# Kernel optimization log

Measured on AMD Instinct MI355X. Metric: run time of the kernel, lower is better.

Reference implementation:

```python
import jax, jax.numpy as jnp
import numpy as np

N, HIDDEN, K = 16384, 256, 5  # k=5 neighbors, first (self) dropped -> 4 hyperedge memberships per node


def _knn_hyperedges(x):
    # Mimics sklearn NearestNeighbors(k=5) + drop self (torch code detaches x here).
    xs = jax.lax.stop_gradient(x)
    n = xs.shape[0]
    sq = jnp.sum(xs * xs, axis=1)
    d2 = sq[:, None] + sq[None, :] - 2.0 * (xs @ xs.T)  # [N, N] squared distances
    d2 = d2.at[jnp.arange(n), jnp.arange(n)].set(jnp.inf)  # exclude self
    _, idx = jax.lax.top_k(-d2, K - 1)  # [N, K-1] nearest neighbors
    node_idx = jnp.repeat(jnp.arange(n), K - 1)  # hyperedge_index[0]: node i
    edge_idx = idx.reshape(-1)                   # hyperedge_index[1]: hyperedge id = neighbor id
    return node_idx, edge_idx


def _prelu(x, a):
    return jnp.where(x >= 0, x, a * x)


def _hconv(x, W, b, node_idx, edge_idx, n):
    # PyG HypergraphConv (heads=1, no attention, unit hyperedge weights):
    # out = D^{-1} H B^{-1} H^T (x W^T) + b
    xt = x @ W.T  # lin has no bias in PyG; bias added at the end
    ones = jnp.ones(node_idx.shape[0], dtype=x.dtype)
    Bdeg = jax.ops.segment_sum(ones, edge_idx, num_segments=n)  # hyperedge degree
    Binv = jnp.where(Bdeg > 0, 1.0 / Bdeg, 0.0)
    Ddeg = jax.ops.segment_sum(ones, node_idx, num_segments=n)  # node degree
    Dinv = jnp.where(Ddeg > 0, 1.0 / Ddeg, 0.0)
    # node -> hyperedge gather/scatter
    e_feat = jax.ops.segment_sum(xt[node_idx], edge_idx, num_segments=n) * Binv[:, None]
    # hyperedge -> node gather/scatter
    out = jax.ops.segment_sum(e_feat[edge_idx], node_idx, num_segments=n) * Dinv[:, None]
    return out + b


def setup_inputs() -> dict:
    key = jax.random.key(0)
    k0, k1, k2, k3 = jax.random.split(key, 4)
    x = jax.random.normal(k0, (N, HIDDEN), dtype=jnp.float32)
    edge_index = jax.random.randint(k1, (2, 65536), 0, N)  # unused by the math, kept per signature
    kaiming = np.sqrt(2.0 / HIDDEN)
    W1 = jax.random.normal(k2, (HIDDEN, HIDDEN), dtype=jnp.float32) * kaiming
    W2 = jax.random.normal(k3, (HIDDEN, HIDDEN), dtype=jnp.float32) * kaiming
    b1 = jnp.zeros((HIDDEN,), dtype=jnp.float32)
    b2 = jnp.zeros((HIDDEN,), dtype=jnp.float32)
    prelu_a = jnp.float32(0.25)  # nn.PReLU() default single shared parameter
    return {"x": x, "edge_index": edge_index, "W1": W1, "b1": b1, "W2": W2, "b2": b2, "prelu_a": prelu_a}


def reference(x, edge_index, W1, b1, W2, b2, prelu_a):
    n = x.shape[0]
    node_idx, edge_idx = _knn_hyperedges(x)
    h = _hconv(x, W1, b1, node_idx, edge_idx, n)
    h = _prelu(h, prelu_a)
    h = _hconv(h, W2, b2, node_idx, edge_idx, n)
    h = h + x  # residual
    return _prelu(h, prelu_a)
```

## Files before the change

### kernel.cpp

```cpp
#include <hip/hip_runtime.h>
#include <stdint.h>

#define NN   16384
#define HID  256
#define LDSK 264
#define NSLICE 16
#define JSL  (NN/NSLICE)
#define JT   32
#define NIT  (JSL/JT)
#define NSETS 4
#define ITILE (NSETS*64)
#define NRS  8
#define GSB  2048
#define NWV  (GSB*4)
#define FLTMAX 3.402823466e38f
#define KEYMAX 0xFFFFFFFFu
#define VBIAS 131072.0f
#define MSTRIDE 17

typedef __attribute__((ext_vector_type(8))) _Float16 f16x8;
typedef __attribute__((ext_vector_type(4))) _Float16 f16x4;
typedef __attribute__((ext_vector_type(4))) float f32x4;

typedef const __attribute__((address_space(1))) unsigned int* gAS1;
typedef __attribute__((address_space(3))) unsigned int* lAS3;

#define NXG (NN*HID/4)
#define NWG (HID*HID/4)
#define CVTB ((NXG + 2*NWG)/256)
__global__ __launch_bounds__(256) void prep_kernel(const float* __restrict__ x,
                                                   const float* __restrict__ W1,
                                                   const float* __restrict__ W2,
                                                   _Float16* __restrict__ xh,
                                                   _Float16* __restrict__ W1h,
                                                   _Float16* __restrict__ W2h,
                                                   float* __restrict__ sqf,
                                                   int* __restrict__ Bdeg){
  #pragma clang fp contract(off)
  int b = blockIdx.x;
  int g0 = b * 256 + threadIdx.x;
  if (g0 < NN) Bdeg[g0] = 0;
  if (b < CVTB){
    int g = g0;
    const float* src; _Float16* dst; int o;
    if (g < NXG)            { src = x;  dst = xh;  o = g; }
    else if (g < NXG + NWG) { src = W1; dst = W1h; o = g - NXG; }
    else                    { src = W2; dst = W2h; o = g - NXG - NWG; }
    float4 v = ((const float4*)src)[o];
    f16x4 h; h.x = (_Float16)v.x; h.y = (_Float16)v.y; h.z = (_Float16)v.z; h.w = (_Float16)v.w;
    ((f16x4*)dst)[o] = h;
  } else {
    int bb = b - CVTB;
    int lane = threadIdx.x & 63;
    int rw   = lane >> 4;
    int h    = (lane >> 3) & 1;
    int j    = lane & 7;
    int row  = (bb * 4 + (threadIdx.x >> 6)) * 4 + rw;
    const float* p = x + (size_t)row * HID + h*128 + j;
    float v0 = p[0];
    float r  = v0 * v0;
    #pragma unroll
    for (int i = 1; i < 16; ++i){ float v = p[i*8]; float m = v * v; r = r + m; }
    float t1 = r  + __shfl_xor(r,  1);
    float t2 = t1 + __shfl_xor(t1, 2);
    float t3 = t2 + __shfl_xor(t2, 4);
    float tot = t3 + __shfl_xor(t3, 8);
    if (h == 0 && j == 0) sqf[row] = tot;
  }
}

__device__ __forceinline__ void load_tile64(unsigned short* dst, const unsigned short* src, int tid){
  const uint4* s = (const uint4*)src;
  #pragma unroll
  for (int r = 0; r < 8; ++r){
    int fl  = tid + (r << 8);
    int row = fl >> 5;
    int c   = fl & 31;
    *(uint4*)&dst[row*LDSK + (c << 3)] = s[fl];
  }
}

__device__ __forceinline__ unsigned umed3(unsigned a, unsigned b, unsigned c){
  unsigned d;
  asm("v_med3_u32 %0, %1, %2, %3" : "=v"(d) : "v"(a), "v"(b), "v"(c));
  return d;
}
__device__ __forceinline__ void ins4(unsigned (&b)[4], unsigned k){
  unsigned b0 = b[0], b1 = b[1], b2 = b[2];
  b[0] = k < b0 ? k : b0;
  b[1] = umed3(k, b0, b1);
  b[2] = umed3(k, b1, b2);
  b[3] = umed3(k, b2, b[3]);
}

__global__ __launch_bounds__(256, 2) void knn_kernel(const _Float16* __restrict__ xh,
                                                     const float* __restrict__ sqf,
                                                     unsigned* __restrict__ candk,
                                                     int ibase){
  __shared__ __align__(16) unsigned short Xj[2][JT*256];
  __shared__ __align__(16) float sqj64[2][JT];

  int tid  = threadIdx.x;
  int sl   = blockIdx.x & (NSLICE-1);
  int i0   = ibase + (blockIdx.x / NSLICE) * ITILE;
  int jb0  = sl * JSL;
  int wave = tid >> 6, lane = tid & 63, quad = lane >> 4, lcol = lane & 15;

  f16x8 bfr[NSETS][8];
  #pragma unroll
  for (int s = 0; s < NSETS; ++s){
    const _Float16* br = xh + (size_t)(i0 + s*64 + wave*16 + lcol) * HID + quad*8;
    #pragma unroll
    for (int ks = 0; ks < 8; ++ks) bfr[s][ks] = *(const f16x8*)(br + ks*32);
  }

  const _Float16* gsrc[4];
  #pragma unroll
  for (int r = 0; r < 4; ++r){
    int m   = r*256 + tid;
    int row = m >> 5;
    int ch  = m & 31;
    gsrc[r] = xh + (size_t)row * HID + ((ch ^ (row & 7)) << 3);
  }

  int b0 = lcol*512 + ((quad ^ (lcol & 3)) << 4) + (((lcol >> 2) & 1) << 6);
  int b1 = b0 ^ 64;

  unsigned bk[NSETS][4];
  #pragma unroll
  for (int s = 0; s < NSETS; ++s)
    #pragma unroll
    for (int e = 0; e < 4; ++e) bk[s][e] = KEYMAX;

  {
    size_t joff = (size_t)jb0 * HID;
    #pragma unroll
    for (int r = 0; r < 4; ++r)
      __builtin_amdgcn_global_load_lds((gAS1)(const void*)(gsrc[r] + joff),
                                       (lAS3)(void*)&Xj[0][(r*256 + tid) * 8],
                                       16, 0, 0);
    if (tid < JT) sqj64[0][tid] = fmaf(sqf[jb0 + tid], 64.f, VBIAS);
  }
  __syncthreads();

  for (int it = 0; it < NIT; ++it){
    if (it + 1 < NIT){
      int nb = (it + 1) & 1;
      int jn = jb0 + (it + 1) * JT;
      size_t joff = (size_t)jn * HID;
      #pragma unroll
      for (int r = 0; r < 4; ++r)
        __builtin_amdgcn_global_load_lds((gAS1)(const void*)(gsrc[r] + joff),
                                         (lAS3)(void*)&Xj[nb][(r*256 + tid) * 8],
                                         16, 0, 0);
      if (tid < JT) sqj64[nb][tid] = fmaf(sqf[jn + tid], 64.f, VBIAS);
    }

    const char*  tb  = (const char*)&Xj[it & 1][0];
    const float* sjb = sqj64[it & 1];
    int jb = jb0 + it * JT;

    #pragma unroll
    for (int sub = 0; sub < 2; ++sub){
      f32x4 acc[NSETS];
      #pragma unroll
      for (int s = 0; s < NSETS; ++s) acc[s] = (f32x4){0.f,0.f,0.f,0.f};
      #pragma unroll
      for (int ks = 0; ks < 8; ++ks){
        f16x8 a = *(const f16x8*)(tb + sub*8192 + ((ks >> 1) << 7) + ((ks & 1) ? b1 : b0));
        #pragma unroll
        for (int s = 0; s < NSETS; ++s)
          acc[s] = __builtin_amdgcn_mfma_f32_16x16x32_f16(a, bfr[s][ks], acc[s], 0, 0, 0);
      }
      float4 sj4 = *(const float4*)&sjb[sub*16 + quad*4];
      int jbase = jb + sub*16 + quad*4;
      #pragma unroll
      for (int reg = 0; reg < 4; ++reg){
        int gj = jbase + reg;
        float sj = (&sj4.x)[reg];
        #pragma unroll
        for (int s = 0; s < NSETS; ++s){
          float v64 = fmaf(-128.f, acc[s][reg], sj);
          unsigned kv = (unsigned)v64;
          unsigned key = (kv << 14) + (unsigned)gj;
          ins4(bk[s], key);
        }
      }
    }
    __syncthreads();
  }

  unsigned* Mk = (unsigned*)Xj;
  #pragma unroll
  for (int s = 0; s < NSETS; ++s){
    int base = (s*64 + wave*16 + lcol)*MSTRIDE + quad*4;
    #pragma unroll
    for (int e = 0; e < 4; ++e) Mk[base+e] = bk[s][e];
  }
  __syncthreads();
  if (tid < ITILE){
    unsigned fk[4];
    #pragma unroll
    for (int e = 0; e < 4; ++e) fk[e] = KEYMAX;
    #pragma unroll
    for (int s = 0; s < 16; ++s) ins4(fk, Mk[tid*MSTRIDE + s]);
    int g = i0 + tid;
    #pragma unroll
    for (int e = 0; e < 4; ++e)
      candk[(size_t)g*(NSLICE*4) + sl*4 + e] = fk[e];
  }
}

__global__ __launch_bounds__(64) void rescore_kernel(const float* __restrict__ x,
                                                     const float* __restrict__ sqf,
                                                     const unsigned* __restrict__ candk,
                                                     int* __restrict__ idx_out,
                                                     int* __restrict__ Bdeg){
  #pragma clang fp contract(off)
  __shared__ float Xi[256];
  __shared__ float Xct[256][NRS+1];
  __shared__ float dex[NRS];
  __shared__ int   sel[NRS];
  int i = blockIdx.x;
  int t = threadIdx.x;
  ((float4*)Xi)[t] = ((const float4*)(x + (size_t)i * HID))[t];
  unsigned kv = candk[(size_t)i*(NSLICE*4) + t];
  if ((kv & 16383u) == (unsigned)i) kv = KEYMAX;
  int rank = 0;
  for (int s = 0; s < 64; ++s){
    unsigned ks = __shfl(kv, s);
    rank += (ks < kv) ? 1 : 0;
  }
  if (rank < NRS) sel[rank] = (int)(kv & 16383u);
  __syncthreads();
  {
    int r = t >> 3, seg = t & 7;
    const float4* src = (const float4*)(x + (size_t)sel[r] * HID);
    #pragma unroll
    for (int m = 0; m < 8; ++m){
      float4 v = src[seg + 8*m];
      int k = 4*(seg + 8*m);
      Xct[k+0][r] = v.x; Xct[k+1][r] = v.y; Xct[k+2][r] = v.z; Xct[k+3][r] = v.w;
    }
  }
  __syncthreads();
  if (t < NRS){
    int j = sel[t];
    float acc = 0.f;
    for (int k = 0; k < 256; ++k) acc = fmaf(Xi[k], Xct[k][t], acc);
    float t1   = sqf[i] + sqf[j];
    float twod = 2.0f * acc;
    dex[t] = t1 - twod;
  }
  __syncthreads();
  if (t == 0){
    unsigned taken = 0;
    #pragma unroll
    for (int k = 0; k < 4; ++k){
      float bdv = FLTMAX; int bj = 0x7fffffff, bs = -1;
      for (int s = 0; s < NRS; ++s){
        if (taken & (1u << s)) continue;
        float d = dex[s]; int j = sel[s];
        if (d < bdv || (d == bdv && j < bj)){ bdv = d; bj = j; bs = s; }
      }
      taken |= 1u << bs;
      idx_out[i*4 + k] = bj;
      atomicAdd(&Bdeg[bj], 1);
    }
  }
}

__global__ __launch_bounds__(256) void gemm_xw(const _Float16* __restrict__ A,
                                               const _Float16* __restrict__ W,
                                               _Float16* __restrict__ out){
  __shared__ unsigned short Ws[64 * LDSK];
  int tid = threadIdx.x;
  int i0 = (blockIdx.x >> 2) * 64;
  int o0 = (blockIdx.x & 3)  * 64;
  int wave = tid >> 6, lane = tid & 63, quad = lane >> 4, lcol = lane & 15;
  load_tile64(Ws, (const unsigned short*)(W + (size_t)o0 * HID), tid);
  f16x8 a[8];
  const _Float16* arow = A + (size_t)(i0 + wave*16 + lcol) * HID + quad*8;
  #pragma unroll
  for (int ks = 0; ks < 8; ++ks) a[ks] = *(const f16x8*)(arow + ks*32);
  __syncthreads();
  #pragma unroll
  for (int sub = 0; sub < 4; ++sub){
    f32x4 acc = {0.f, 0.f, 0.f, 0.f};
    #pragma unroll
    for (int ks = 0; ks < 8; ++ks){
      f16x8 b = *(const f16x8*)&Ws[(sub*16 + lcol)*LDSK + quad*8 + ks*32];
      acc = __builtin_amdgcn_mfma_f32_16x16x32_f16(a[ks], b, acc, 0, 0, 0);
    }
    #pragma unroll
    for (int reg = 0; reg < 4; ++reg)
      out[(size_t)(i0 + wave*16 + quad*4 + reg)*HID + o0 + sub*16 + lcol] = (_Float16)acc[reg];
  }
}

__global__ __launch_bounds__(256) void prefix_kernel(const int* __restrict__ Bdeg,
                                                     int* __restrict__ off,
                                                     int* __restrict__ cursor){
  __shared__ int psum[256];
  __shared__ int excl[256];
  int t = threadIdx.x;
  int base = t * 64;
  int s = 0;
  for (int k = 0; k < 64; ++k) s += Bdeg[base + k];
  psum[t] = s;
  __syncthreads();
  if (t == 0){ int a = 0; for (int k = 0; k < 256; ++k){ excl[k] = a; a += psum[k]; } }
  __syncthreads();
  int a = excl[t];
  for (int k = 0; k < 64; ++k){ int dv = Bdeg[base + k]; off[base+k] = a; cursor[base+k] = a; a += dv; }
}

__global__ __launch_bounds__(256) void fill_kernel(const int* __restrict__ idx,
                                                   int* __restrict__ cursor,
                                                   int* __restrict__ rev){
  int i = blockIdx.x * 256 + threadIdx.x;
  #pragma unroll
  for (int t = 0; t < 4; ++t){
    int e = idx[i*4 + t];
    int p = atomicAdd(&cursor[e], 1);
    rev[p] = i;
  }
}

__global__ __launch_bounds__(256) void efeat_kernel(const _Float16* __restrict__ xt,
                                                    const int* __restrict__ off,
                                                    const int* __restrict__ deg,
                                                    const int* __restrict__ rev,
                                                    _Float16* __restrict__ E){
  int wv   = blockIdx.x * 4 + (threadIdx.x >> 6);
  int lane = threadIdx.x & 63;
  for (int e = wv; e < NN; e += NWV){
    int o = off[e], d = deg[e];
    float s0 = 0.f, s1 = 0.f, s2 = 0.f, s3 = 0.f;
    #pragma unroll 4
    for (int k = 0; k < d; ++k){
      int node = rev[o + k];
      f16x4 v = *(const f16x4*)(xt + (size_t)node * HID + lane * 4);
      s0 += (float)v.x; s1 += (float)v.y; s2 += (float)v.z; s3 += (float)v.w;
    }
    f16x4 w;
    if (d > 0){
      float fd = (float)d;
      w.x = (_Float16)(s0 / fd); w.y = (_Float16)(s1 / fd);
      w.z = (_Float16)(s2 / fd); w.w = (_Float16)(s3 / fd);
    } else {
      w.x = (_Float16)0.f; w.y = (_Float16)0.f; w.z = (_Float16)0.f; w.w = (_Float16)0.f;
    }
    *(f16x4*)(E + (size_t)e * HID + lane * 4) = w;
  }
}

__global__ __launch_bounds__(256) void fin1_kernel(const _Float16* __restrict__ E,
                                                   const int* __restrict__ idx,
                                                   const float* __restrict__ b1,
                                                   const float* __restrict__ pa,
                                                   _Float16* __restrict__ h1){
  int wv   = blockIdx.x * 4 + (threadIdx.x >> 6);
  int lane = threadIdx.x & 63;
  float4 bc = ((const float4*)b1)[lane];
  float a   = pa[0];
  for (int i = wv; i < NN; i += NWV){
    const int* ip = idx + i*4;
    int e0 = ip[0], e1 = ip[1], e2 = ip[2], e3 = ip[3];
    f16x4 v0 = *(const f16x4*)(E + (size_t)e0*HID + lane*4);
    f16x4 v1 = *(const f16x4*)(E + (size_t)e1*HID + lane*4);
    f16x4 v2 = *(const f16x4*)(E + (size_t)e2*HID + lane*4);
    f16x4 v3 = *(const f16x4*)(E + (size_t)e3*HID + lane*4);
    f16x4 w;
    #pragma unroll
    for (int c = 0; c < 4; ++c){
      float s = ((float)v0[c] + (float)v1[c] + (float)v2[c] + (float)v3[c]);
      float acc = 0.25f * s + (&bc.x)[c];
      acc = (acc >= 0.f) ? acc : a * acc;
      w[c] = (_Float16)acc;
    }
    *(f16x4*)(h1 + (size_t)i*HID + lane*4) = w;
  }
}

__global__ __launch_bounds__(256) void fin2_kernel(const _Float16* __restrict__ E,
                                                   const int* __restrict__ idx,
                                                   const float* __restrict__ b2,
                                                   const float* __restrict__ x,
                                                   const float* __restrict__ pa,
                                                   float* __restrict__ out){
  int wv   = blockIdx.x * 4 + (threadIdx.x >> 6);
  int lane = threadIdx.x & 63;
  float4 bc = ((const float4*)b2)[lane];
  float a   = pa[0];
  for (int i = wv; i < NN; i += NWV){
    const int* ip = idx + i*4;
    int e0 = ip[0], e1 = ip[1], e2 = ip[2], e3 = ip[3];
    f16x4 v0 = *(const f16x4*)(E + (size_t)e0*HID + lane*4);
    f16x4 v1 = *(const f16x4*)(E + (size_t)e1*HID + lane*4);
    f16x4 v2 = *(const f16x4*)(E + (size_t)e2*HID + lane*4);
    f16x4 v3 = *(const f16x4*)(E + (size_t)e3*HID + lane*4);
    float4 xr = *(const float4*)(x + (size_t)i*HID + lane*4);
    float4 w;
    #pragma unroll
    for (int c = 0; c < 4; ++c){
      float s = ((float)v0[c] + (float)v1[c] + (float)v2[c] + (float)v3[c]);
      float acc = 0.25f * s + (&bc.x)[c] + (&xr.x)[c];
      acc = (acc >= 0.f) ? acc : a * acc;
      (&w.x)[c] = acc;
    }
    *(float4*)(out + (size_t)i*HID + lane*4) = w;
  }
}

extern "C" void kernel_launch(void* const* d_in, const int* in_sizes, int n_in,
                              void* d_out, int out_size, void* d_ws, size_t ws_size,
                              hipStream_t stream){
  (void)in_sizes; (void)n_in; (void)out_size; (void)ws_size;
  const float* x  = (const float*)d_in[0];
  const float* W1 = (const float*)d_in[2];
  const float* b1 = (const float*)d_in[3];
  const float* W2 = (const float*)d_in[4];
  const float* b2 = (const float*)d_in[5];
  const float* pa = (const float*)d_in[6];
  float* out = (float*)d_out;

  char* ws = (char*)d_ws;
  float*  sqf    = (float*) (ws + 0);
  int*    idx    = (int*)   (ws + 65536);
  int*    Bdeg   = (int*)   (ws + 327680);
  int*    offE   = (int*)   (ws + 393216);
  int*    cursor = (int*)   (ws + 458752);
  int*    rev    = (int*)   (ws + 524288);
  _Float16* xh   = (_Float16*)(ws + (size_t)(5<<20));
  _Float16* W1h  = (_Float16*)(ws + (size_t)(13<<20));
  _Float16* W2h  = (_Float16*)(ws + (size_t)(13<<20) + 131072);
  _Float16* xt   = (_Float16*)(ws + (size_t)(13<<20) + 262144);
  _Float16* E    = (_Float16*)(ws + (size_t)(21<<20) + 262144);
  _Float16* h1   = (_Float16*)(ws + (size_t)(29<<20) + 262144);
  unsigned* candk = (unsigned*)xt;

  prep_kernel   <<<CVTB + NN/16, 256, 0, stream>>>(x, W1, W2, xh, W1h, W2h, sqf, Bdeg);
  knn_kernel    <<<(NN/ITILE/2)*NSLICE, 256, 0, stream>>>(xh, sqf, candk, 0);
  knn_kernel    <<<(NN/ITILE/2)*NSLICE, 256, 0, stream>>>(xh, sqf, candk, NN/2);
  rescore_kernel<<<NN, 64, 0, stream>>>(x, sqf, candk, idx, Bdeg);
  prefix_kernel <<<1, 256, 0, stream>>>(Bdeg, offE, cursor);
  fill_kernel   <<<NN/256, 256, 0, stream>>>(idx, cursor, rev);

  gemm_xw       <<<(NN/64)*4, 256, 0, stream>>>(xh, W1h, xt);
  efeat_kernel  <<<GSB, 256, 0, stream>>>(xt, offE, Bdeg, rev, E);
  fin1_kernel   <<<GSB, 256, 0, stream>>>(E, idx, b1, pa, h1);

  gemm_xw       <<<(NN/64)*4, 256, 0, stream>>>(h1, W2h, xt);
  efeat_kernel  <<<GSB, 256, 0, stream>>>(xt, offE, Bdeg, rev, E);
  fin2_kernel   <<<GSB, 256, 0, stream>>>(E, idx, b2, x, pa, out);
}
```

Measured before the change: 451.4 us.

## Merge kNN launches, preload squared norms, use explicit waitcnt and barriers

The two half-range kNN launches become one launch over all rows. The squared-norm slice for the block's j-range is loaded into LDS once up front instead of per tile. The __syncthreads calls are replaced by explicit s_waitcnt vmcnt/lgkmcnt plus s_barrier and sched_barrier, so the prefetch of the next tile can stay in flight while the current tile is computed. This removes one launch and some per-iteration synchronisation cost, but the hand-counted vmcnt(4) is fragile: it is only correct if exactly four global loads per thread are outstanding.

```diff
diff --git a/kernel.cpp b/kernel.cpp
--- a/kernel.cpp
+++ b/kernel.cpp
@@ -95,14 +95,13 @@
 
 __global__ __launch_bounds__(256, 2) void knn_kernel(const _Float16* __restrict__ xh,
                                                      const float* __restrict__ sqf,
-                                                     unsigned* __restrict__ candk,
-                                                     int ibase){
+                                                     unsigned* __restrict__ candk){
   __shared__ __align__(16) unsigned short Xj[2][JT*256];
-  __shared__ __align__(16) float sqj64[2][JT];
+  __shared__ __align__(16) float sqjA[JSL];
 
   int tid  = threadIdx.x;
   int sl   = blockIdx.x & (NSLICE-1);
-  int i0   = ibase + (blockIdx.x / NSLICE) * ITILE;
+  int i0   = (blockIdx.x / NSLICE) * ITILE;
   int jb0  = sl * JSL;
   int wave = tid >> 6, lane = tid & 63, quad = lane >> 4, lcol = lane & 15;
 
@@ -133,19 +132,26 @@
     for (int e = 0; e < 4; ++e) bk[s][e] = KEYMAX;
 
   {
+    float4 sv = ((const float4*)(sqf + jb0))[tid];
+    float4 sw;
+    sw.x = fmaf(sv.x, 64.f, VBIAS); sw.y = fmaf(sv.y, 64.f, VBIAS);
+    sw.z = fmaf(sv.z, 64.f, VBIAS); sw.w = fmaf(sv.w, 64.f, VBIAS);
+    ((float4*)sqjA)[tid] = sw;
     size_t joff = (size_t)jb0 * HID;
     #pragma unroll
     for (int r = 0; r < 4; ++r)
       __builtin_amdgcn_global_load_lds((gAS1)(const void*)(gsrc[r] + joff),
                                        (lAS3)(void*)&Xj[0][(r*256 + tid) * 8],
                                        16, 0, 0);
-    if (tid < JT) sqj64[0][tid] = fmaf(sqf[jb0 + tid], 64.f, VBIAS);
-  }
-  __syncthreads();
+    asm volatile("s_waitcnt vmcnt(0) lgkmcnt(0)" ::: "memory");
+  }
+  __builtin_amdgcn_s_barrier();
+  __builtin_amdgcn_sched_barrier(0);
 
   for (int it = 0; it < NIT; ++it){
+    int cur = it & 1;
     if (it + 1 < NIT){
-      int nb = (it + 1) & 1;
+      int nb = cur ^ 1;
       int jn = jb0 + (it + 1) * JT;
       size_t joff = (size_t)jn * HID;
       #pragma unroll
@@ -153,11 +159,15 @@
         __builtin_amdgcn_global_load_lds((gAS1)(const void*)(gsrc[r] + joff),
                                          (lAS3)(void*)&Xj[nb][(r*256 + tid) * 8],
                                          16, 0, 0);
-      if (tid < JT) sqj64[nb][tid] = fmaf(sqf[jn + tid], 64.f, VBIAS);
-    }
-
-    const char*  tb  = (const char*)&Xj[it & 1][0];
-    const float* sjb = sqj64[it & 1];
+      asm volatile("s_waitcnt vmcnt(4)" ::: "memory");
+    } else {
+      asm volatile("s_waitcnt vmcnt(0)" ::: "memory");
+    }
+    __builtin_amdgcn_s_barrier();
+    __builtin_amdgcn_sched_barrier(0);
+
+    const char*  tb  = (const char*)&Xj[cur][0];
+    const float* sjb = &sqjA[it * JT];
     int jb = jb0 + it * JT;
 
     #pragma unroll
@@ -187,7 +197,9 @@
         }
       }
     }
-    __syncthreads();
+    asm volatile("s_waitcnt lgkmcnt(0)" ::: "memory");
+    __builtin_amdgcn_s_barrier();
+    __builtin_amdgcn_sched_barrier(0);
   }
 
   unsigned* Mk = (unsigned*)Xj;
@@ -441,8 +453,7 @@
   unsigned* candk = (unsigned*)xt;
 
   prep_kernel   <<<CVTB + NN/16, 256, 0, stream>>>(x, W1, W2, xh, W1h, W2h, sqf, Bdeg);
-  knn_kernel    <<<(NN/ITILE/2)*NSLICE, 256, 0, stream>>>(xh, sqf, candk, 0);
-  knn_kernel    <<<(NN/ITILE/2)*NSLICE, 256, 0, stream>>>(xh, sqf, candk, NN/2);
+  knn_kernel    <<<(NN/ITILE)*NSLICE, 256, 0, stream>>>(xh, sqf, candk);
   rescore_kernel<<<NN, 64, 0, stream>>>(x, sqf, candk, idx, Bdeg);
   prefix_kernel <<<1, 256, 0, stream>>>(Bdeg, offE, cursor);
   fill_kernel   <<<NN/256, 256, 0, stream>>>(idx, cursor, rev);
```

Measured after the change: 437.0 us. -3.2%, faster.
